# Kernel tuning notes

Measured on AMD Instinct MI355X. Metric: run time of the kernel, lower is better.

Reference implementation:

```python
import jax, jax.numpy as jnp
import numpy as np

NHEAD = 16
EPS_L1 = 1e-12
LN_EPS = 1e-5


def _layernorm(x, g, b):
    mu = jnp.mean(x, axis=-1, keepdims=True)
    var = jnp.mean(jnp.square(x - mu), axis=-1, keepdims=True)
    return (x - mu) / jnp.sqrt(var + LN_EPS) * g + b


def setup_inputs() -> dict:
    key = jax.random.key(0)
    ks = jax.random.split(key, 16)
    S, B, E, P, F = 2048, 2, 1024, 64, 4096
    sc = lambda n: 1.0 / np.sqrt(n)
    return {
        "src": jax.random.normal(ks[0], (S, B, E), jnp.float32),
        "pos_embed": jax.random.normal(ks[1], (B, P, S), jnp.float32),
        "in_proj_w": jax.random.normal(ks[2], (3 * E, E), jnp.float32) * sc(E),
        "in_proj_b": jnp.zeros((3 * E,), jnp.float32),
        "out_w": jax.random.normal(ks[3], (E, E), jnp.float32) * sc(E),
        "out_b": jnp.zeros((E,), jnp.float32),
        "lin1_w": jax.random.normal(ks[4], (F, E), jnp.float32) * sc(E),
        "lin1_b": jnp.zeros((F,), jnp.float32),
        "lin2_w": jax.random.normal(ks[5], (E, F), jnp.float32) * sc(F),
        "lin2_b": jnp.zeros((E,), jnp.float32),
        "ln1_g": jnp.ones((E,), jnp.float32),
        "ln1_b": jnp.zeros((E,), jnp.float32),
        "ln2_g": jnp.ones((E,), jnp.float32),
        "ln2_b": jnp.zeros((E,), jnp.float32),
        "pos_w": jax.random.normal(ks[6], (P, P), jnp.float32) * sc(P),
        "pos_b": jnp.zeros((P,), jnp.float32),
    }


def reference(src, pos_embed, in_proj_w, in_proj_b, out_w, out_b,
              lin1_w, lin1_b, lin2_w, lin2_b,
              ln1_g, ln1_b, ln2_g, ln2_b, pos_w, pos_b):
    S, B, E = src.shape
    H = NHEAD
    Dh = E // H

    # --- custom positional-similarity kernel (cosine_similarity w/ L1 norm) ---
    pe = jnp.einsum('bps,qp->bqs', pos_embed, pos_w) + pos_b[None, :, None]  # learnable pos
    l1 = jnp.maximum(jnp.sum(jnp.abs(pe), axis=1, keepdims=True), EPS_L1)
    pe = pe / l1                                                # [B,P,S]
    pos_sim = jnp.einsum('bps,bpt->bst', pe, pe)                # [B,S,S]

    # --- manual multi-head self-attention ---
    qkv = src @ in_proj_w.T + in_proj_b                          # [S,B,3E]
    q, k, v = jnp.split(qkv, 3, axis=-1)
    q = q * (Dh ** -0.5)
    to_bhsd = lambda t: jnp.transpose(t.reshape(S, B, H, Dh), (1, 2, 0, 3))
    q, k, v = to_bhsd(q), to_bhsd(k), to_bhsd(v)                 # [B,H,S,Dh]
    scores = jnp.einsum('bhsd,bhtd->bhst', q, k) + pos_sim[:, None]
    attn = jax.nn.softmax(scores, axis=-1)                       # [B,H,S,S]
    ctx = jnp.einsum('bhst,bhtd->bhsd', attn, v)                 # [B,H,S,Dh]
    ctx = jnp.transpose(ctx, (2, 0, 1, 3)).reshape(S, B, E)
    attn_out = ctx @ out_w.T + out_b

    # --- residual + norm + FFN (post-norm, relu) ---
    x = _layernorm(src + attn_out, ln1_g, ln1_b)
    ff = jax.nn.relu(x @ lin1_w.T + lin1_b) @ lin2_w.T + lin2_b
    return _layernorm(x + ff, ln2_g, ln2_b)
```

## Files before the change

### kernel.cpp

```cpp
#include <hip/hip_runtime.h>
#include <hip/hip_bf16.h>
#include <math.h>

#define S_LEN 2048
#define BATCH 2
#define EMB   1024
#define NH    16
#define DH    64
#define E3    3072
#define FF    4096
#define PP    64

typedef __bf16 bf16x8 __attribute__((ext_vector_type(8)));
typedef float  floatx4 __attribute__((ext_vector_type(4)));

__device__ __forceinline__ void load_lds16(const void* g, void* l) {
  __builtin_amdgcn_global_load_lds(
      (const __attribute__((address_space(1))) void*)g,
      (__attribute__((address_space(3))) void*)l, 16, 0, 0);
}

__global__ __launch_bounds__(256) void cvt_kernel(
    const float* __restrict__ in, __hip_bfloat16* __restrict__ out, int n)
{
  int i = (blockIdx.x * 256 + threadIdx.x) * 8;
  if (i >= n) return;
  float4 a = *(const float4*)&in[i];
  float4 b = *(const float4*)&in[i + 4];
  __hip_bfloat16 t[8];
  t[0] = __float2bfloat16(a.x); t[1] = __float2bfloat16(a.y);
  t[2] = __float2bfloat16(a.z); t[3] = __float2bfloat16(a.w);
  t[4] = __float2bfloat16(b.x); t[5] = __float2bfloat16(b.y);
  t[6] = __float2bfloat16(b.z); t[7] = __float2bfloat16(b.w);
  *(float4*)&out[i] = *(float4*)t;
}

__global__ __launch_bounds__(64) void pe_kernel(
    const float* __restrict__ pos_embed, const float* __restrict__ pos_w,
    const float* __restrict__ pos_b, __hip_bfloat16* __restrict__ peT)
{
  __shared__ float pw[PP * PP];
  int tid = threadIdx.x;
  for (int i = 0; i < PP; ++i) pw[i * PP + tid] = pos_w[i * PP + tid];
  __syncthreads();
  int s = blockIdx.x * 64 + tid;
  int b = blockIdx.y;
  float acc[PP];
#pragma unroll
  for (int q = 0; q < PP; ++q) acc[q] = pos_b[q];
  for (int p = 0; p < PP; ++p) {
    float x = pos_embed[(size_t)(b * PP + p) * S_LEN + s];
#pragma unroll
    for (int q = 0; q < PP; ++q) acc[q] += pw[q * PP + p] * x;
  }
  float l1 = 0.f;
#pragma unroll
  for (int q = 0; q < PP; ++q) l1 += fabsf(acc[q]);
  float inv = 1.f / fmaxf(l1, 1e-12f);
  __hip_bfloat16 tmp[PP];
#pragma unroll
  for (int q = 0; q < PP; ++q) tmp[q] = __float2bfloat16(acc[q] * inv);
  float4* dst = (float4*)&peT[((size_t)b * S_LEN + s) * PP];
#pragma unroll
  for (int i = 0; i < 8; ++i) dst[i] = ((float4*)tmp)[i];
}

template <int WR, int WC>
__global__ __launch_bounds__(256) void gemm_bf16(
    const __hip_bfloat16* __restrict__ A, const __hip_bfloat16* __restrict__ W,
    const float* __restrict__ bias, float* __restrict__ Cf,
    __hip_bfloat16* __restrict__ Cb, int M, int N, int K, int relu, int qkscale,
    long strideA, long strideW, long strideC)
{
  constexpr int BM = 2 * WR * 16;
  constexpr int BN = 2 * WC * 16;
  __shared__ __bf16 As[BM * 64];
  __shared__ __bf16 Bs[BN * 64];
  A += (size_t)blockIdx.z * strideA;
  W += (size_t)blockIdx.z * strideW;
  int tid = threadIdx.x;
  int bm = blockIdx.y * BM;
  int bn = blockIdx.x * BN;
  int wave = tid >> 6, lane = tid & 63;
  int wm = (wave & 1) * (WR * 16), wn = (wave >> 1) * (WC * 16);
  int srow = tid >> 3, scb = tid & 7;
  int gcb = scb ^ (srow & 7);
  const __hip_bfloat16* Ap = A + (size_t)(bm + srow) * K + gcb * 8;
  const __hip_bfloat16* Wp = W + (size_t)(bn + srow) * K + gcb * 8;
  __bf16* AsBase = As + tid * 8;
  __bf16* BsBase = Bs + tid * 8;
  int r15 = lane & 15, quad = lane >> 4;

  floatx4 acc[WR * WC];
#pragma unroll
  for (int i = 0; i < WR * WC; ++i) acc[i] = (floatx4){0.f, 0.f, 0.f, 0.f};

  for (int k0 = 0; k0 < K; k0 += 64) {
    __syncthreads();
#pragma unroll
    for (int io = 0; io < BM / 32; ++io)
      load_lds16(Ap + (size_t)(32 * io) * K + k0, AsBase + io * 2048);
#pragma unroll
    for (int io = 0; io < BN / 32; ++io)
      load_lds16(Wp + (size_t)(32 * io) * K + k0, BsBase + io * 2048);
    __syncthreads();
#pragma unroll
    for (int kc = 0; kc < 2; ++kc) {
      bf16x8 af[WR], bfv[WC];
      int kb = kc * 4 + quad;
#pragma unroll
      for (int i = 0; i < WR; ++i) {
        int rowa = wm + i * 16 + r15;
        af[i] = *(const bf16x8*)&As[rowa * 64 + (kb ^ (rowa & 7)) * 8];
      }
#pragma unroll
      for (int j = 0; j < WC; ++j) {
        int rowb = wn + j * 16 + r15;
        bfv[j] = *(const bf16x8*)&Bs[rowb * 64 + (kb ^ (rowb & 7)) * 8];
      }
#pragma unroll
      for (int i = 0; i < WR; ++i)
#pragma unroll
        for (int j = 0; j < WC; ++j)
          acc[i * WC + j] = __builtin_amdgcn_mfma_f32_16x16x32_bf16(
              af[i], bfv[j], acc[i * WC + j], 0, 0, 0);
    }
  }
  int crow0 = bm + wm + quad * 4;
  int ccol0 = bn + wn + r15;
  float* CfB = Cf ? Cf + (size_t)blockIdx.z * strideC : nullptr;
  __hip_bfloat16* CbB = Cb ? Cb + (size_t)blockIdx.z * strideC : nullptr;
#pragma unroll
  for (int j = 0; j < WC; ++j) {
    int col = ccol0 + j * 16;
    float bv = bias ? bias[col] : 0.f;
    float scale = (qkscale && col < EMB) ? 0.125f : 1.f;
#pragma unroll
    for (int i = 0; i < WR; ++i) {
#pragma unroll
      for (int r = 0; r < 4; ++r) {
        int row = crow0 + i * 16 + r;
        float v = (acc[i * WC + j][r] + bv) * scale;
        if (relu) v = fmaxf(v, 0.f);
        if (CfB) CfB[(size_t)row * N + col] = v;
        if (CbB) CbB[(size_t)row * N + col] = __float2bfloat16(v);
      }
    }
  }
}

__global__ __launch_bounds__(256) void transpose_v(
    const __hip_bfloat16* __restrict__ qkv, __hip_bfloat16* __restrict__ vT)
{
  __shared__ __hip_bfloat16 tile[64][72];
  int c0 = blockIdx.x * 64, t0 = blockIdx.y * 64, b = blockIdx.z;
  int tid = threadIdx.x;
#pragma unroll
  for (int i = 0; i < 2; ++i) {
    int k = tid * 2 + i;
    int row = k >> 3, col = (k & 7) * 8;
    float4 v = *(const float4*)&qkv[((size_t)(t0 + row) * BATCH + b) * E3 + 2 * EMB + c0 + col];
    __hip_bfloat16 tmp[8];
    *(float4*)tmp = v;
#pragma unroll
    for (int j = 0; j < 8; ++j) tile[row][col + j] = tmp[j];
  }
  __syncthreads();
#pragma unroll
  for (int i = 0; i < 2; ++i) {
    int k = tid * 2 + i;
    int crow = k >> 3, tcol = (k & 7) * 8;
    __hip_bfloat16 tmp[8];
#pragma unroll
    for (int j = 0; j < 8; ++j) tmp[j] = tile[tcol + j][crow];
    *(float4*)&vT[((size_t)(b * EMB + c0 + crow)) * S_LEN + t0 + tcol] = *(float4*)tmp;
  }
}

__global__ __launch_bounds__(256) void attn_mfma(
    const __hip_bfloat16* __restrict__ qkv,
    const __hip_bfloat16* __restrict__ vT,
    const __hip_bfloat16* __restrict__ peT,
    __hip_bfloat16* __restrict__ ctx)
{
  __shared__ __bf16 Ks[2][4096];
  __shared__ __bf16 Kp[2][4096];
  __shared__ __bf16 Vs[2][4096];
  __shared__ __bf16 Ps[8192];
  int tid = threadIdx.x;
  int q0 = blockIdx.x * 128, h = blockIdx.y, b = blockIdx.z;
  int w = tid >> 6, lane = tid & 63, quad = lane >> 4, r15 = lane & 15;
  int srow = tid >> 3, scb = tid & 7;
  int x7 = r15 & 7;

  const __hip_bfloat16* kbase = qkv + EMB + (size_t)h * DH;
  const __hip_bfloat16* vbase = vT + ((size_t)b * EMB + h * DH) * S_LEN;
  const __hip_bfloat16* pbase = peT + (size_t)b * S_LEN * PP;

  bf16x8 qa[2][4];
#pragma unroll
  for (int qb = 0; qb < 2; ++qb) {
    int qrow = q0 + w * 32 + qb * 16 + r15;
#pragma unroll
    for (int kc = 0; kc < 2; ++kc)
      qa[qb][kc] = *(const bf16x8*)&qkv[
          ((size_t)qrow * BATCH + b) * E3 + h * DH + kc * 32 + quad * 8];
#pragma unroll
    for (int kc = 0; kc < 2; ++kc)
      qa[qb][2 + kc] = *(const bf16x8*)&pbase[
          (size_t)qrow * PP + kc * 32 + quad * 8];
  }

#pragma unroll
  for (int i = 0; i < 2; ++i) {
    int row = i * 32 + srow;
    int gcb = scb ^ (row & 7);
    load_lds16(kbase + ((size_t)row * BATCH + b) * E3 + gcb * 8,
               Ks[0] + i * 2048 + tid * 8);
    load_lds16(pbase + (size_t)row * PP + gcb * 8,
               Kp[0] + i * 2048 + tid * 8);
    load_lds16(vbase + (size_t)row * S_LEN + gcb * 8,
               Vs[0] + i * 2048 + tid * 8);
  }
  __syncthreads();

  floatx4 of[2][4];
#pragma unroll
  for (int qb = 0; qb < 2; ++qb)
#pragma unroll
    for (int j = 0; j < 4; ++j) of[qb][j] = (floatx4){0.f, 0.f, 0.f, 0.f};
  float lp[2] = {0.f, 0.f};

  __bf16* pw0 = Ps + (w * 2 + 0) * 1024;
  __bf16* pw1 = Ps + (w * 2 + 1) * 1024;

  for (int kt = 0; kt < 32; ++kt) {
    int cur = kt & 1;
    int t0 = kt * 64;
    if (kt < 31) {
      int tn = t0 + 64;
      int nb = cur ^ 1;
#pragma unroll
      for (int i = 0; i < 2; ++i) {
        int row = i * 32 + srow;
        int gcb = scb ^ (row & 7);
        load_lds16(kbase + ((size_t)(tn + row) * BATCH + b) * E3 + gcb * 8,
                   Ks[nb] + i * 2048 + tid * 8);
        load_lds16(pbase + (size_t)(tn + row) * PP + gcb * 8,
                   Kp[nb] + i * 2048 + tid * 8);
        load_lds16(vbase + (size_t)row * S_LEN + tn + gcb * 8,
                   Vs[nb] + i * 2048 + tid * 8);
      }
    }

    floatx4 sf[2][4];
#pragma unroll
    for (int qb = 0; qb < 2; ++qb)
#pragma unroll
      for (int j = 0; j < 4; ++j) sf[qb][j] = (floatx4){0.f, 0.f, 0.f, 0.f};
#pragma unroll
    for (int j = 0; j < 4; ++j) {
      int rowk = j * 16 + r15;
      int rx = rowk & 7;
      bf16x8 kf0 = *(const bf16x8*)&Ks[cur][rowk * 64 + ((quad ^ rx)) * 8];
      bf16x8 kf1 = *(const bf16x8*)&Ks[cur][rowk * 64 + (((4 + quad) ^ rx)) * 8];
      bf16x8 kp0 = *(const bf16x8*)&Kp[cur][rowk * 64 + ((quad ^ rx)) * 8];
      bf16x8 kp1 = *(const bf16x8*)&Kp[cur][rowk * 64 + (((4 + quad) ^ rx)) * 8];
#pragma unroll
      for (int qb = 0; qb < 2; ++qb) {
        sf[qb][j] = __builtin_amdgcn_mfma_f32_16x16x32_bf16(kf0, qa[qb][0], sf[qb][j], 0, 0, 0);
        sf[qb][j] = __builtin_amdgcn_mfma_f32_16x16x32_bf16(kf1, qa[qb][1], sf[qb][j], 0, 0, 0);
        sf[qb][j] = __builtin_amdgcn_mfma_f32_16x16x32_bf16(kp0, qa[qb][2], sf[qb][j], 0, 0, 0);
        sf[qb][j] = __builtin_amdgcn_mfma_f32_16x16x32_bf16(kp1, qa[qb][3], sf[qb][j], 0, 0, 0);
      }
    }

#pragma unroll
    for (int qb = 0; qb < 2; ++qb) {
      __bf16* pwq = qb ? pw1 : pw0;
#pragma unroll
      for (int j = 0; j < 4; ++j) {
        float e0 = __expf(fminf(sf[qb][j][0], 60.f));
        float e1 = __expf(fminf(sf[qb][j][1], 60.f));
        float e2 = __expf(fminf(sf[qb][j][2], 60.f));
        float e3 = __expf(fminf(sf[qb][j][3], 60.f));
        lp[qb] += (e0 + e1) + (e2 + e3);
        __hip_bfloat16 t4[4];
        t4[0] = __float2bfloat16(e0); t4[1] = __float2bfloat16(e1);
        t4[2] = __float2bfloat16(e2); t4[3] = __float2bfloat16(e3);
        int addr = r15 * 64 + (((j * 2 + (quad >> 1)) ^ x7) * 8) + (quad & 1) * 4;
        *(float2*)&pwq[addr] = *(float2*)t4;
      }
    }
    __asm__ volatile("s_waitcnt lgkmcnt(0)" ::: "memory");

    bf16x8 pb00 = *(const bf16x8*)&pw0[r15 * 64 + ((quad ^ x7) * 8)];
    bf16x8 pb01 = *(const bf16x8*)&pw0[r15 * 64 + (((4 + quad) ^ x7) * 8)];
    bf16x8 pb10 = *(const bf16x8*)&pw1[r15 * 64 + ((quad ^ x7) * 8)];
    bf16x8 pb11 = *(const bf16x8*)&pw1[r15 * 64 + (((4 + quad) ^ x7) * 8)];
#pragma unroll
    for (int jd = 0; jd < 4; ++jd) {
      int rowd = jd * 16 + r15;
      bf16x8 vb0 = *(const bf16x8*)&Vs[cur][rowd * 64 + (quad ^ (rowd & 7)) * 8];
      bf16x8 vb1 = *(const bf16x8*)&Vs[cur][rowd * 64 + ((4 + quad) ^ (rowd & 7)) * 8];
      of[0][jd] = __builtin_amdgcn_mfma_f32_16x16x32_bf16(vb0, pb00, of[0][jd], 0, 0, 0);
      of[0][jd] = __builtin_amdgcn_mfma_f32_16x16x32_bf16(vb1, pb01, of[0][jd], 0, 0, 0);
      of[1][jd] = __builtin_amdgcn_mfma_f32_16x16x32_bf16(vb0, pb10, of[1][jd], 0, 0, 0);
      of[1][jd] = __builtin_amdgcn_mfma_f32_16x16x32_bf16(vb1, pb11, of[1][jd], 0, 0, 0);
    }
    __syncthreads();
  }

#pragma unroll
  for (int qb = 0; qb < 2; ++qb) {
    float l = lp[qb];
    l += __shfl_xor(l, 16, 64);
    l += __shfl_xor(l, 32, 64);
    float inv = 1.f / l;
    size_t rbase = ((size_t)(q0 + w * 32 + qb * 16 + r15) * BATCH + b) * EMB + h * DH;
#pragma unroll
    for (int jd = 0; jd < 4; ++jd) {
      __hip_bfloat16 o4[4];
      o4[0] = __float2bfloat16(of[qb][jd][0] * inv);
      o4[1] = __float2bfloat16(of[qb][jd][1] * inv);
      o4[2] = __float2bfloat16(of[qb][jd][2] * inv);
      o4[3] = __float2bfloat16(of[qb][jd][3] * inv);
      *(float2*)&ctx[rbase + jd * 16 + quad * 4] = *(float2*)o4;
    }
  }
}

__global__ __launch_bounds__(256) void ln_kernel(
    const float* __restrict__ x1, const float* __restrict__ x2,
    const float* __restrict__ g, const float* __restrict__ bb,
    float* __restrict__ out, __hip_bfloat16* __restrict__ out_bf)
{
  int row = blockIdx.x;
  int tid = threadIdx.x;
  const float* p1 = x1 + (size_t)row * EMB;
  const float* p2 = x2 + (size_t)row * EMB;
  float4 v1 = *(const float4*)&p1[tid * 4];
  float4 v2 = *(const float4*)&p2[tid * 4];
  float x[4] = {v1.x + v2.x, v1.y + v2.y, v1.z + v2.z, v1.w + v2.w};
  float s = x[0] + x[1] + x[2] + x[3];
  float s2 = x[0] * x[0] + x[1] * x[1] + x[2] * x[2] + x[3] * x[3];
#pragma unroll
  for (int off = 32; off >= 1; off >>= 1) {
    s  += __shfl_xor(s, off, 64);
    s2 += __shfl_xor(s2, off, 64);
  }
  __shared__ float ws1[4], ws2[4];
  int wid = tid >> 6, lane = tid & 63;
  if (lane == 0) { ws1[wid] = s; ws2[wid] = s2; }
  __syncthreads();
  s  = ws1[0] + ws1[1] + ws1[2] + ws1[3];
  s2 = ws2[0] + ws2[1] + ws2[2] + ws2[3];
  float mean = s * (1.f / EMB);
  float var  = s2 * (1.f / EMB) - mean * mean;
  float inv  = rsqrtf(var + 1e-5f);
  float4 gv = *(const float4*)&g[tid * 4];
  float4 bv = *(const float4*)&bb[tid * 4];
  float4 o;
  o.x = (x[0] - mean) * inv * gv.x + bv.x;
  o.y = (x[1] - mean) * inv * gv.y + bv.y;
  o.z = (x[2] - mean) * inv * gv.z + bv.z;
  o.w = (x[3] - mean) * inv * gv.w + bv.w;
  *(float4*)&out[(size_t)row * EMB + tid * 4] = o;
  if (out_bf) {
    __hip_bfloat16 t[4];
    t[0] = __float2bfloat16(o.x); t[1] = __float2bfloat16(o.y);
    t[2] = __float2bfloat16(o.z); t[3] = __float2bfloat16(o.w);
    *(float2*)&out_bf[(size_t)row * EMB + tid * 4] = *(float2*)t;
  }
}

extern "C" void kernel_launch(void* const* d_in, const int* in_sizes, int n_in,
                              void* d_out, int out_size, void* d_ws, size_t ws_size,
                              hipStream_t stream)
{
  const float* src       = (const float*)d_in[0];
  const float* pos_embed = (const float*)d_in[1];
  const float* in_proj_w = (const float*)d_in[2];
  const float* in_proj_b = (const float*)d_in[3];
  const float* out_w     = (const float*)d_in[4];
  const float* out_b     = (const float*)d_in[5];
  const float* lin1_w    = (const float*)d_in[6];
  const float* lin1_b    = (const float*)d_in[7];
  const float* lin2_w    = (const float*)d_in[8];
  const float* lin2_b    = (const float*)d_in[9];
  const float* ln1_g     = (const float*)d_in[10];
  const float* ln1_b     = (const float*)d_in[11];
  const float* ln2_g     = (const float*)d_in[12];
  const float* ln2_b     = (const float*)d_in[13];
  const float* pos_w     = (const float*)d_in[14];
  const float* pos_b     = (const float*)d_in[15];
  float* out = (float*)d_out;
  float* ws  = (float*)d_ws;

  __hip_bfloat16* peT    = (__hip_bfloat16*)ws;
  __hip_bfloat16* qkv_bf = (__hip_bfloat16*)(ws + 8519680);
  __hip_bfloat16* vT_bf  = (__hip_bfloat16*)(ws + 14811136);
  __hip_bfloat16* src_bf = (__hip_bfloat16*)(ws + 16908288);
  __hip_bfloat16* inw_bf  = (__hip_bfloat16*)(ws + 19005440);
  __hip_bfloat16* outw_bf = (__hip_bfloat16*)(ws + 20578304);
  __hip_bfloat16* ctx_bf = (__hip_bfloat16*)(ws + 21102592);
  __hip_bfloat16* l1w_bf = (__hip_bfloat16*)(ws + 23199744);
  __hip_bfloat16* l2w_bf = (__hip_bfloat16*)(ws + 25296896);
  float* proj            = ws + 27394048;
  __hip_bfloat16* x_bf   = (__hip_bfloat16*)ws + 2097152;
  float* xbuf            = ws + 2097152 + 2097152 / 1;
  x_bf = (__hip_bfloat16*)ws;
  xbuf = ws + 2097152;
  __hip_bfloat16* h1_bf  = (__hip_bfloat16*)(ws + 6291456);

  const int M = S_LEN * BATCH;

  cvt_kernel<<<4194304 / 2048, 256, 0, stream>>>(src, src_bf, 4194304);
  cvt_kernel<<<3145728 / 2048, 256, 0, stream>>>(in_proj_w, inw_bf, 3145728);
  cvt_kernel<<<1048576 / 2048, 256, 0, stream>>>(out_w, outw_bf, 1048576);
  cvt_kernel<<<4194304 / 2048, 256, 0, stream>>>(lin1_w, l1w_bf, 4194304);
  cvt_kernel<<<4194304 / 2048, 256, 0, stream>>>(lin2_w, l2w_bf, 4194304);
  pe_kernel<<<dim3(S_LEN / 64, BATCH), 64, 0, stream>>>(pos_embed, pos_w, pos_b, peT);
  gemm_bf16<4, 4><<<dim3(E3 / 128, M / 128, 1), 256, 0, stream>>>(
      src_bf, inw_bf, in_proj_b, nullptr, qkv_bf, M, E3, EMB, 0, 1, 0, 0, 0);
  transpose_v<<<dim3(EMB / 64, S_LEN / 64, BATCH), 256, 0, stream>>>(qkv_bf, vT_bf);
  attn_mfma<<<dim3(S_LEN / 128, NH, BATCH), 256, 0, stream>>>(
      qkv_bf, vT_bf, peT, ctx_bf);
  gemm_bf16<2, 4><<<dim3(EMB / 128, M / 64, 1), 256, 0, stream>>>(
      ctx_bf, outw_bf, out_b, proj, nullptr, M, EMB, EMB, 0, 0, 0, 0, 0);
  ln_kernel<<<dim3(M), 256, 0, stream>>>(src, proj, ln1_g, ln1_b, xbuf, x_bf);
  gemm_bf16<4, 4><<<dim3(FF / 128, M / 128, 1), 256, 0, stream>>>(
      x_bf, l1w_bf, lin1_b, nullptr, h1_bf, M, FF, EMB, 1, 0, 0, 0, 0);
  gemm_bf16<2, 4><<<dim3(EMB / 128, M / 64, 1), 256, 0, stream>>>(
      h1_bf, l2w_bf, lin2_b, proj, nullptr, M, EMB, FF, 0, 0, 0, 0, 0);
  ln_kernel<<<dim3(M), 256, 0, stream>>>(xbuf, proj, ln2_g, ln2_b, out, nullptr);
}
```

Before: 437.8 us.

## Add 256x256 phased MFMA GEMM for QKV and FFN1 projections

Adds a new GEMM kernel with 256x256 block tiles and 8 waves. It uses XOR-swizzled LDS, direct global-to-LDS loads, double buffering, and a four-phase MFMA schedule with barriers and s_setprio, interleaving loads with compute. The QKV and FFN1 GEMMs now use it to get more reuse per loaded byte and better overlap of memory and math. The grids get smaller (192 and 256 blocks), which may leave some CUs idle, and the larger register and LDS footprint per block lowers occupancy.

```diff
diff --git a/kernel.cpp b/kernel.cpp
--- a/kernel.cpp
+++ b/kernel.cpp
@@ -144,6 +144,173 @@
         if (relu) v = fmaxf(v, 0.f);
         if (CfB) CfB[(size_t)row * N + col] = v;
         if (CbB) CbB[(size_t)row * N + col] = __float2bfloat16(v);
+      }
+    }
+  }
+}
+
+__global__ __launch_bounds__(512, 2) void gemm256_bf16(
+    const __hip_bfloat16* __restrict__ A, const __hip_bfloat16* __restrict__ W,
+    const float* __restrict__ bias, __hip_bfloat16* __restrict__ Cb,
+    int M, int N, int K, int relu, int qkscale)
+{
+  __shared__ __bf16 As[2][16384];
+  __shared__ __bf16 Bs[2][16384];
+  const int tid = threadIdx.x;
+  const int bm = blockIdx.y * 256;
+  const int bn = blockIdx.x * 256;
+  const int wave = tid >> 6, lane = tid & 63;
+  const int wm = (wave >> 2) * 128, wn = (wave & 3) * 64;
+  const int r15 = lane & 15, quad = lane >> 4;
+  const int srow = tid >> 3, scb = tid & 7;
+  const int NT = K >> 6;
+
+  const __hip_bfloat16* Ap = A + (size_t)bm * K;
+  const __hip_bfloat16* Wp = W + (size_t)bn * K;
+
+  auto stageA = [&](int buf, int k0, int h) {
+#pragma unroll
+    for (int io = 0; io < 2; ++io) {
+      int row = h * 128 + io * 64 + srow;
+      int gcb = scb ^ (row & 7);
+      load_lds16(Ap + (size_t)row * K + k0 + gcb * 8,
+                 &As[buf][(h * 128 + io * 64) * 64] + tid * 8);
+    }
+  };
+  auto stageB = [&](int buf, int k0, int h) {
+#pragma unroll
+    for (int io = 0; io < 2; ++io) {
+      int row = h * 128 + io * 64 + srow;
+      int gcb = scb ^ (row & 7);
+      load_lds16(Wp + (size_t)row * K + k0 + gcb * 8,
+                 &Bs[buf][(h * 128 + io * 64) * 64] + tid * 8);
+    }
+  };
+
+  floatx4 acc[8][4];
+#pragma unroll
+  for (int i = 0; i < 8; ++i)
+#pragma unroll
+    for (int jn = 0; jn < 4; ++jn) acc[i][jn] = (floatx4){0.f, 0.f, 0.f, 0.f};
+
+  stageA(0, 0, 0); stageA(0, 0, 1);
+  stageB(0, 0, 0); stageB(0, 0, 1);
+  stageA(1, 64, 0); stageA(1, 64, 1);
+  asm volatile("s_waitcnt vmcnt(4)" ::: "memory");
+  __builtin_amdgcn_s_barrier();
+  __builtin_amdgcn_sched_barrier(0);
+
+#define PHASE_BAR() do { __builtin_amdgcn_sched_barrier(0); \
+                         __builtin_amdgcn_s_barrier();      \
+                         __builtin_amdgcn_sched_barrier(0); } while (0)
+
+  bf16x8 af[4][2], bfr[4][2];
+  for (int j = 0; j < NT; ++j) {
+    const int cur = j & 1, nxt = cur ^ 1;
+    const int k1 = (j + 1) << 6, k2 = (j + 2) << 6;
+
+#pragma unroll
+    for (int i = 0; i < 4; ++i) {
+      int row = wm + i * 16 + r15;
+#pragma unroll
+      for (int kc = 0; kc < 2; ++kc)
+        af[i][kc] = *(const bf16x8*)&As[cur][row * 64 + (((kc * 4 + quad) ^ (row & 7)) * 8)];
+    }
+#pragma unroll
+    for (int jn = 0; jn < 2; ++jn) {
+      int row = wn + jn * 16 + r15;
+#pragma unroll
+      for (int kc = 0; kc < 2; ++kc)
+        bfr[jn][kc] = *(const bf16x8*)&Bs[cur][row * 64 + (((kc * 4 + quad) ^ (row & 7)) * 8)];
+    }
+    if (j + 1 < NT) stageB(nxt, k1, 0);
+    PHASE_BAR();
+    __builtin_amdgcn_s_setprio(1);
+#pragma unroll
+    for (int i = 0; i < 4; ++i)
+#pragma unroll
+      for (int jn = 0; jn < 2; ++jn)
+#pragma unroll
+        for (int kc = 0; kc < 2; ++kc)
+          acc[i][jn] = __builtin_amdgcn_mfma_f32_16x16x32_bf16(
+              af[i][kc], bfr[jn][kc], acc[i][jn], 0, 0, 0);
+    __builtin_amdgcn_s_setprio(0);
+    PHASE_BAR();
+
+#pragma unroll
+    for (int jn = 2; jn < 4; ++jn) {
+      int row = wn + jn * 16 + r15;
+#pragma unroll
+      for (int kc = 0; kc < 2; ++kc)
+        bfr[jn][kc] = *(const bf16x8*)&Bs[cur][row * 64 + (((kc * 4 + quad) ^ (row & 7)) * 8)];
+    }
+    if (j + 1 < NT) stageB(nxt, k1, 1);
+    PHASE_BAR();
+    __builtin_amdgcn_s_setprio(1);
+#pragma unroll
+    for (int i = 0; i < 4; ++i)
+#pragma unroll
+      for (int jn = 2; jn < 4; ++jn)
+#pragma unroll
+        for (int kc = 0; kc < 2; ++kc)
+          acc[i][jn] = __builtin_amdgcn_mfma_f32_16x16x32_bf16(
+              af[i][kc], bfr[jn][kc], acc[i][jn], 0, 0, 0);
+    __builtin_amdgcn_s_setprio(0);
+    PHASE_BAR();
+
+#pragma unroll
+    for (int i = 0; i < 4; ++i) {
+      int row = wm + (i + 4) * 16 + r15;
+#pragma unroll
+      for (int kc = 0; kc < 2; ++kc)
+        af[i][kc] = *(const bf16x8*)&As[cur][row * 64 + (((kc * 4 + quad) ^ (row & 7)) * 8)];
+    }
+    PHASE_BAR();
+    __builtin_amdgcn_s_setprio(1);
+#pragma unroll
+    for (int i = 0; i < 4; ++i)
+#pragma unroll
+      for (int jn = 2; jn < 4; ++jn)
+#pragma unroll
+        for (int kc = 0; kc < 2; ++kc)
+          acc[i + 4][jn] = __builtin_amdgcn_mfma_f32_16x16x32_bf16(
+              af[i][kc], bfr[jn][kc], acc[i + 4][jn], 0, 0, 0);
+    __builtin_amdgcn_s_setprio(0);
+    PHASE_BAR();
+
+    if (j + 2 < NT) { stageA(cur, k2, 0); stageA(cur, k2, 1); }
+    if (j < NT - 2) asm volatile("s_waitcnt vmcnt(4)" ::: "memory");
+    else            asm volatile("s_waitcnt vmcnt(0)" ::: "memory");
+    PHASE_BAR();
+    __builtin_amdgcn_s_setprio(1);
+#pragma unroll
+    for (int i = 0; i < 4; ++i)
+#pragma unroll
+      for (int jn = 0; jn < 2; ++jn)
+#pragma unroll
+        for (int kc = 0; kc < 2; ++kc)
+          acc[i + 4][jn] = __builtin_amdgcn_mfma_f32_16x16x32_bf16(
+              af[i][kc], bfr[jn][kc], acc[i + 4][jn], 0, 0, 0);
+    __builtin_amdgcn_s_setprio(0);
+    PHASE_BAR();
+  }
+#undef PHASE_BAR
+
+  const int crow0 = bm + wm + quad * 4;
+  const int ccol0 = bn + wn + r15;
+#pragma unroll
+  for (int jn = 0; jn < 4; ++jn) {
+    int col = ccol0 + jn * 16;
+    float bv = bias ? bias[col] : 0.f;
+    float scale = (qkscale && col < EMB) ? 0.125f : 1.f;
+#pragma unroll
+    for (int i = 0; i < 8; ++i) {
+#pragma unroll
+      for (int r = 0; r < 4; ++r) {
+        int row = crow0 + i * 16 + r;
+        float v = (acc[i][jn][r] + bv) * scale;
+        if (relu) v = fmaxf(v, 0.f);
+        Cb[(size_t)row * N + col] = __float2bfloat16(v);
       }
     }
   }
@@ -407,10 +574,8 @@
   __hip_bfloat16* l1w_bf = (__hip_bfloat16*)(ws + 23199744);
   __hip_bfloat16* l2w_bf = (__hip_bfloat16*)(ws + 25296896);
   float* proj            = ws + 27394048;
-  __hip_bfloat16* x_bf   = (__hip_bfloat16*)ws + 2097152;
-  float* xbuf            = ws + 2097152 + 2097152 / 1;
-  x_bf = (__hip_bfloat16*)ws;
-  xbuf = ws + 2097152;
+  __hip_bfloat16* x_bf   = (__hip_bfloat16*)ws;
+  float* xbuf            = ws + 2097152;
   __hip_bfloat16* h1_bf  = (__hip_bfloat16*)(ws + 6291456);
 
   const int M = S_LEN * BATCH;
@@ -421,16 +586,16 @@
   cvt_kernel<<<4194304 / 2048, 256, 0, stream>>>(lin1_w, l1w_bf, 4194304);
   cvt_kernel<<<4194304 / 2048, 256, 0, stream>>>(lin2_w, l2w_bf, 4194304);
   pe_kernel<<<dim3(S_LEN / 64, BATCH), 64, 0, stream>>>(pos_embed, pos_w, pos_b, peT);
-  gemm_bf16<4, 4><<<dim3(E3 / 128, M / 128, 1), 256, 0, stream>>>(
-      src_bf, inw_bf, in_proj_b, nullptr, qkv_bf, M, E3, EMB, 0, 1, 0, 0, 0);
+  gemm256_bf16<<<dim3(E3 / 256, M / 256), 512, 0, stream>>>(
+      src_bf, inw_bf, in_proj_b, qkv_bf, M, E3, EMB, 0, 1);
   transpose_v<<<dim3(EMB / 64, S_LEN / 64, BATCH), 256, 0, stream>>>(qkv_bf, vT_bf);
   attn_mfma<<<dim3(S_LEN / 128, NH, BATCH), 256, 0, stream>>>(
       qkv_bf, vT_bf, peT, ctx_bf);
   gemm_bf16<2, 4><<<dim3(EMB / 128, M / 64, 1), 256, 0, stream>>>(
       ctx_bf, outw_bf, out_b, proj, nullptr, M, EMB, EMB, 0, 0, 0, 0, 0);
   ln_kernel<<<dim3(M), 256, 0, stream>>>(src, proj, ln1_g, ln1_b, xbuf, x_bf);
-  gemm_bf16<4, 4><<<dim3(FF / 128, M / 128, 1), 256, 0, stream>>>(
-      x_bf, l1w_bf, lin1_b, nullptr, h1_bf, M, FF, EMB, 1, 0, 0, 0, 0);
+  gemm256_bf16<<<dim3(FF / 256, M / 256), 512, 0, stream>>>(
+      x_bf, l1w_bf, lin1_b, h1_bf, M, FF, EMB, 1, 0);
   gemm_bf16<2, 4><<<dim3(EMB / 128, M / 64, 1), 256, 0, stream>>>(
       h1_bf, l2w_bf, lin2_b, proj, nullptr, M, EMB, FF, 0, 0, 0, 0, 0);
   ln_kernel<<<dim3(M), 256, 0, stream>>>(xbuf, proj, ln2_g, ln2_b, out, nullptr);
```

After: 441.5 us. No clear change (+0.8%).
